# Kernel optimization log

Hardware: AMD Instinct MI355X
Metric: run time of the kernel (lower is better)

## Reference

```python
import jax, jax.numpy as jnp
import numpy as np

K = 9          # kernel_size (number of neighbors), dilation=1
EPS_IN = 1e-5  # InstanceNorm2d eps
EPS_NORM = 1e-12  # F.normalize eps


def instance_norm(x):
    # InstanceNorm2d(affine=False): per-sample, per-channel normalization (biased var)
    m = x.mean(axis=(2, 3), keepdims=True)
    v = x.var(axis=(2, 3), keepdims=True)
    return (x - m) * jax.lax.rsqrt(v + EPS_IN)


def conv1x1(x, w, b):
    # x: [B,C,H,W], w: [O,C], b: [O]
    return jnp.einsum('bchw,oc->bohw', x, w) + b[None, :, None, None]


def setup_inputs() -> dict:
    key = jax.random.key(0)
    ks = jax.random.split(key, 5)
    B, C, H, W = 8, 96, 56, 56
    s = lambda fan_in: 1.0 / np.sqrt(fan_in)
    return {
        'x': jax.random.normal(ks[0], (B, C, H, W), jnp.float32),
        'fc1_w': jax.random.normal(ks[1], (C, C), jnp.float32) * s(C),
        'fc1_b': jnp.zeros((C,), jnp.float32),
        'gconv_w': jax.random.normal(ks[2], (2 * C, 2 * C), jnp.float32) * s(2 * C),
        'gconv_b': jnp.zeros((2 * C,), jnp.float32),
        'fc2_w': jax.random.normal(ks[3], (C, 2 * C), jnp.float32) * s(2 * C),
        'fc2_b': jnp.zeros((C,), jnp.float32),
    }


def reference(x, fc1_w, fc1_b, gconv_w, gconv_b, fc2_w, fc2_b):
    B, C, H, W = x.shape
    N = H * W
    shortcut = x

    # fc1: Conv2d 1x1 + InstanceNorm2d
    h = instance_norm(conv1x1(x, fc1_w, fc1_b))

    # flatten spatial -> nodes: [B,N,C]
    feats = h.reshape(B, C, N).transpose(0, 2, 1)

    # DenseDilatedKnnGraph: l2-normalize features, squared-euclidean pairwise distance, top-k nearest
    nrm = feats / jnp.maximum(jnp.linalg.norm(feats, axis=-1, keepdims=True), EPS_NORM)
    sq = jnp.sum(nrm * nrm, axis=-1)                       # [B,N]
    dist = sq[:, :, None] - 2.0 * jnp.einsum('bnc,bmc->bnm', nrm, nrm) + sq[:, None, :]
    _, nn_idx = jax.lax.top_k(-dist, K)                    # [B,N,K] neighbor indices (edge_index[0])

    # EdgeConv2d: x_i = center features, x_j = gathered neighbor features (unnormalized fc1 output)
    x_i = feats[:, :, None, :]                             # [B,N,1,C]
    x_j = jax.vmap(lambda f, i: f[i])(feats, nn_idx)       # [B,N,K,C]
    edge = jnp.concatenate(
        [jnp.broadcast_to(x_i, x_j.shape), x_j - x_i], axis=-1)  # [B,N,K,2C]

    # BasicConv([2C, 2C], act='relu', norm=None): conv1x1 + bias + relu, then max over neighbors
    e = jax.nn.relu(jnp.einsum('bnkc,oc->bnko', edge, gconv_w) + gconv_b)
    agg = e.max(axis=2)                                    # [B,N,2C]
    g = agg.transpose(0, 2, 1).reshape(B, 2 * C, H, W)

    # fc2: Conv2d 1x1 (2C->C) + InstanceNorm2d, residual
    out = instance_norm(conv1x1(g, fc2_w, fc2_b)) + shortcut
    return out
```

## Files before the change

kernel.cpp:

```cpp
#include <hip/hip_runtime.h>
#include <float.h>

#define BQ 8
#define CHN 96
#define NP 3136
#define KNN 9
#define C2 192
#define NT 196
#define MCH 4
#define TPC (NT/MCH)
#define NFRAG 9
#define NLIST 16

typedef __attribute__((ext_vector_type(8))) short bf16x8;
typedef __attribute__((ext_vector_type(4))) float f32x4;

__device__ inline ushort f2bf(float x) {
  unsigned u = __float_as_uint(x);
  return (ushort)((u + 0x7FFFu + ((u >> 16) & 1u)) >> 16);
}
__device__ inline float bf2f(ushort h) { return __uint_as_float((unsigned)h << 16); }

__global__ __launch_bounds__(256) void k1_conv1(const float* __restrict__ x,
    const float* __restrict__ w, const float* __restrict__ bias, float* __restrict__ h) {
  __shared__ float sw[CHN * CHN];
  __shared__ float sx[CHN][64];
  int b = blockIdx.y;
  int n0 = blockIdx.x * 64;
  int tid = threadIdx.x;
  for (int i = tid; i < CHN * CHN; i += 256) sw[i] = w[i];
  const float* xb = x + (size_t)b * CHN * NP + n0;
  for (int i = tid; i < CHN * 64; i += 256) {
    int c = i >> 6, nn = i & 63;
    sx[c][nn] = xb[(size_t)c * NP + nn];
  }
  __syncthreads();
  int nn = tid & 63;
  int o0 = (tid >> 6) * 24;
  float acc[24];
#pragma unroll
  for (int j = 0; j < 24; ++j) acc[j] = 0.f;
  for (int c = 0; c < CHN; ++c) {
    float xv = sx[c][nn];
#pragma unroll
    for (int j = 0; j < 24; ++j) acc[j] = fmaf(sw[(o0 + j) * CHN + c], xv, acc[j]);
  }
  float* hb = h + (size_t)b * CHN * NP + n0;
#pragma unroll
  for (int j = 0; j < 24; ++j) hb[(size_t)(o0 + j) * NP + nn] = acc[j] + bias[o0 + j];
}

__global__ __launch_bounds__(256) void k2_stats(const float* __restrict__ src,
                                                float* __restrict__ stat) {
  int bo = blockIdx.x;
  const float* p = src + (size_t)bo * NP;
  float s = 0.f, ss = 0.f;
  for (int i = threadIdx.x; i < NP; i += 256) { float v = p[i]; s += v; ss = fmaf(v, v, ss); }
#pragma unroll
  for (int off = 32; off; off >>= 1) { s += __shfl_down(s, off); ss += __shfl_down(ss, off); }
  __shared__ float as[4], ass[4];
  int wv = threadIdx.x >> 6;
  if ((threadIdx.x & 63) == 0) { as[wv] = s; ass[wv] = ss; }
  __syncthreads();
  if (threadIdx.x == 0) {
    float S = as[0] + as[1] + as[2] + as[3];
    float SS = ass[0] + ass[1] + ass[2] + ass[3];
    float mean = S * (1.f / NP);
    float var = SS * (1.f / NP) - mean * mean;
    if (var < 0.f) var = 0.f;
    stat[bo * 2] = mean;
    stat[bo * 2 + 1] = 1.f / sqrtf(var + 1e-5f);
  }
}

__global__ __launch_bounds__(256) void k3_norm(const float* __restrict__ h,
    const float* __restrict__ stat, float* __restrict__ feats, float* __restrict__ nrm,
    float* __restrict__ sq) {
  __shared__ float tile[CHN][33];
  __shared__ float part[8][32];
  __shared__ float sinv[32];
  int b = blockIdx.y, n0 = blockIdx.x * 32;
  int tid = threadIdx.x;
  for (int i = tid; i < CHN * 32; i += 256) {
    int c = i >> 5, nn = i & 31;
    float m = stat[(b * CHN + c) * 2];
    float r = stat[(b * CHN + c) * 2 + 1];
    tile[c][nn] = (h[((size_t)(b * CHN + c)) * NP + n0 + nn] - m) * r;
  }
  __syncthreads();
  int nn = tid & 31, sub = tid >> 5;
  float ss = 0.f;
#pragma unroll
  for (int j = 0; j < 12; ++j) { float f = tile[sub * 12 + j][nn]; ss = fmaf(f, f, ss); }
  part[sub][nn] = ss;
  __syncthreads();
  if (tid < 32) {
    float S = 0.f;
#pragma unroll
    for (int w = 0; w < 8; ++w) S += part[w][tid];
    float norm = sqrtf(S);
    sinv[tid] = 1.f / fmaxf(norm, 1e-12f);
  }
  __syncthreads();
  float inv = sinv[nn];
  float ss2 = 0.f;
#pragma unroll
  for (int j = 0; j < 12; ++j) { float f = tile[sub * 12 + j][nn] * inv; ss2 = fmaf(f, f, ss2); }
  part[sub][nn] = ss2;
  __syncthreads();
  if (tid < 32) {
    float S = 0.f;
#pragma unroll
    for (int w = 0; w < 8; ++w) S += part[w][tid];
    sq[(size_t)b * NP + n0 + tid] = S;
  }
  for (int i = tid; i < 32 * CHN; i += 256) {
    int nn2 = i / CHN, c = i - nn2 * CHN;
    float f = tile[c][nn2];
    size_t o = ((size_t)b * NP + n0 + nn2) * CHN + c;
    feats[o] = f;
    nrm[o] = f * sinv[nn2];
  }
}

__global__ __launch_bounds__(256) void k3b_prep(const float* __restrict__ nrm,
    ushort* __restrict__ ast, ushort* __restrict__ bst) {
  int b = blockIdx.y, t = blockIdx.x;
  int tid = threadIdx.x;
  const float* nb = nrm + (size_t)b * NP * CHN;
  ushort* ao = ast + (((size_t)b * NT + t) * NFRAG) * 512;
  for (int e = tid; e < NFRAG * 512; e += 256) {
    int f = e >> 9, l = (e >> 3) & 63, j = e & 7;
    int part = f / 3, sl = f - part * 3;
    int c = sl * 32 + (l >> 4) * 8 + j;
    int m = t * 16 + (l & 15);
    float xv = nb[(size_t)m * CHN + c];
    ushort hh = f2bf(xv);
    float rm = xv - bf2f(hh);
    ushort md = f2bf(rm);
    ushort v = (part == 0) ? hh : (part == 1) ? md : f2bf(rm - bf2f(md));
    ao[e] = v;
  }
  ushort* bo = bst + (((size_t)b * NT + t) * NFRAG) * 512;
  for (int e = tid; e < NFRAG * 512; e += 256) {
    int f = e >> 9, l = (e >> 3) & 63, j = e & 7;
    int part = f / 3, sl = f - part * 3;
    int c = sl * 32 + (l >> 4) * 8 + j;
    int n = t * 16 + (l & 15);
    float y = -2.f * nb[(size_t)n * CHN + c];
    ushort hh = f2bf(y);
    float rm = y - bf2f(hh);
    ushort md = f2bf(rm);
    ushort v = (part == 0) ? hh : (part == 1) ? md : f2bf(rm - bf2f(md));
    bo[e] = v;
  }
}

#define CSWAP(vI, iI, vJ, iJ) do { \
    bool _s = (vJ) < (vI); \
    float _fa = _s ? (vJ) : (vI); float _fb = _s ? (vI) : (vJ); \
    int _ia = _s ? (iJ) : (iI); int _ib = _s ? (iI) : (iJ); \
    (vI) = _fa; (vJ) = _fb; (iI) = _ia; (iJ) = _ib; \
  } while (0)

__global__ __launch_bounds__(256) void k4_mfma(
    const ushort* __restrict__ ast, const ushort* __restrict__ bst,
    const float* __restrict__ sq, float* __restrict__ pd, int* __restrict__ pi,
    int chunk0) {
  int b = blockIdx.z, chunk = blockIdx.y + chunk0, ng = blockIdx.x;
  int wave = threadIdx.x >> 6, lane = threadIdx.x & 63;
  int tn = ng * 4 + wave;

  __shared__ ushort lds_b[4 * NFRAG * 512];
  {
    const bf16x8* bp = (const bf16x8*)(bst + (((size_t)b * NT + tn) * NFRAG) * 512);
    bf16x8* dst = (bf16x8*)(lds_b + wave * (NFRAG * 512));
#pragma unroll
    for (int f = 0; f < NFRAG; ++f) dst[f * 64 + lane] = bp[f * 64 + lane];
  }
  const bf16x8* bl = (const bf16x8*)(lds_b + wave * (NFRAG * 512));

  const float* sqb = sq + (size_t)b * NP;
  const ushort* astb = ast + ((size_t)b * NT) * (NFRAG * 512);
  int t0 = chunk * TPC;
  const size_t TS = (size_t)NFRAG * 512;

  float tv0 = FLT_MAX, tv1 = FLT_MAX, tv2 = FLT_MAX, tv3 = FLT_MAX, tv4 = FLT_MAX;
  float tv5 = FLT_MAX, tv6 = FLT_MAX, tv7 = FLT_MAX, tv8 = FLT_MAX;
  int ti0 = 0x7fffffff, ti1 = 0x7fffffff, ti2 = 0x7fffffff, ti3 = 0x7fffffff;
  int ti4 = 0x7fffffff, ti5 = 0x7fffffff, ti6 = 0x7fffffff, ti7 = 0x7fffffff;
  int ti8 = 0x7fffffff;

  for (int tl = 0; tl < TPC; ++tl) {
    const bf16x8* ap = (const bf16x8*)(astb + (size_t)(t0 + tl) * TS);
    bf16x8 aH0 = ap[0 * 64 + lane], aH1 = ap[1 * 64 + lane], aH2 = ap[2 * 64 + lane];
    bf16x8 aM0 = ap[3 * 64 + lane], aM1 = ap[4 * 64 + lane], aM2 = ap[5 * 64 + lane];
    bf16x8 aL0 = ap[6 * 64 + lane], aL1 = ap[7 * 64 + lane], aL2 = ap[8 * 64 + lane];
    int mbase = (t0 + tl) * 16 + ((lane >> 4) << 2);
    float4 sqv = *(const float4*)(sqb + mbase);
    f32x4 acc0 = {0.f, 0.f, 0.f, 0.f}, acc1 = {0.f, 0.f, 0.f, 0.f};
    f32x4 acc2 = {0.f, 0.f, 0.f, 0.f}, acc3 = {0.f, 0.f, 0.f, 0.f};
#pragma unroll
    for (int s = 0; s < 3; ++s) {
      bf16x8 aH = (s == 0) ? aH0 : (s == 1) ? aH1 : aH2;
      bf16x8 aM = (s == 0) ? aM0 : (s == 1) ? aM1 : aM2;
      bf16x8 aL = (s == 0) ? aL0 : (s == 1) ? aL1 : aL2;
      bf16x8 bH = bl[(0 + s) * 64 + lane];
      bf16x8 bM = bl[(3 + s) * 64 + lane];
      bf16x8 bL = bl[(6 + s) * 64 + lane];
      acc0 = __builtin_amdgcn_mfma_f32_16x16x32_bf16(aH, bH, acc0, 0, 0, 0);
      acc1 = __builtin_amdgcn_mfma_f32_16x16x32_bf16(aM, bH, acc1, 0, 0, 0);
      acc2 = __builtin_amdgcn_mfma_f32_16x16x32_bf16(aL, bH, acc2, 0, 0, 0);
      acc3 = __builtin_amdgcn_mfma_f32_16x16x32_bf16(aH, bM, acc3, 0, 0, 0);
      acc2 = __builtin_amdgcn_mfma_f32_16x16x32_bf16(aH, bL, acc2, 0, 0, 0);
      acc3 = __builtin_amdgcn_mfma_f32_16x16x32_bf16(aM, bM, acc3, 0, 0, 0);
    }
#pragma unroll
    for (int r = 0; r < 4; ++r) {
      float d = (((acc1[r] + acc3[r]) + acc2[r]) + acc0[r]) + sqv[r];
      int m = mbase + r;
      if (d < tv8) {
        tv8 = d; ti8 = m;
        CSWAP(tv7, ti7, tv8, ti8);
        CSWAP(tv6, ti6, tv7, ti7);
        CSWAP(tv5, ti5, tv6, ti6);
        CSWAP(tv4, ti4, tv5, ti5);
        CSWAP(tv3, ti3, tv4, ti4);
        CSWAP(tv2, ti2, tv3, ti3);
        CSWAP(tv1, ti1, tv2, ti2);
        CSWAP(tv0, ti0, tv1, ti1);
      }
    }
  }
  int g = lane >> 4;
  int n = tn * 16 + (lane & 15);
  size_t base = (((size_t)b * NLIST + (chunk * 4 + g)) * NP + n) * (size_t)KNN;
  pd[base + 0] = tv0; pi[base + 0] = ti0;
  pd[base + 1] = tv1; pi[base + 1] = ti1;
  pd[base + 2] = tv2; pi[base + 2] = ti2;
  pd[base + 3] = tv3; pi[base + 3] = ti3;
  pd[base + 4] = tv4; pi[base + 4] = ti4;
  pd[base + 5] = tv5; pi[base + 5] = ti5;
  pd[base + 6] = tv6; pi[base + 6] = ti6;
  pd[base + 7] = tv7; pi[base + 7] = ti7;
  pd[base + 8] = tv8; pi[base + 8] = ti8;
}

#define ARGMIN4(e0, j0, e1, j1, e2, j2, e3, j3, DW, IW, W0, W1, W2, W3) \
  bool _l01 = ((e0) < (e1)) || ((e0) == (e1) && (j0) < (j1)); \
  float _da = _l01 ? (e0) : (e1); int _ia = _l01 ? (j0) : (j1); \
  bool _l23 = ((e2) < (e3)) || ((e2) == (e3) && (j2) < (j3)); \
  float _db = _l23 ? (e2) : (e3); int _ib = _l23 ? (j2) : (j3); \
  bool _lab = (_da < _db) || (_da == _db && _ia < _ib); \
  float DW = _lab ? _da : _db; int IW = _lab ? _ia : _ib; \
  bool W0 = _lab && _l01, W1 = _lab && !_l01, W2 = !_lab && _l23, W3 = !_lab && !_l23;

__global__ __launch_bounds__(256) void k4b_merge(const float* __restrict__ pd,
    const int* __restrict__ pi, int* __restrict__ nidx) {
  __shared__ float ld_d[256][KNN];
  __shared__ int   ld_i[256][KNN];
  int tid = threadIdx.x;
  int gid = blockIdx.x * 256 + tid;
  int q = gid >> 2, s = gid & 3;
  int b = q / NP, n = q - b * NP;
  size_t b0 = (((size_t)b * NLIST + (s * 4 + 0)) * NP + n) * (size_t)KNN;
  size_t b1 = (((size_t)b * NLIST + (s * 4 + 1)) * NP + n) * (size_t)KNN;
  size_t b2 = (((size_t)b * NLIST + (s * 4 + 2)) * NP + n) * (size_t)KNN;
  size_t b3 = (((size_t)b * NLIST + (s * 4 + 3)) * NP + n) * (size_t)KNN;
  int p0 = 0, p1 = 0, p2 = 0, p3 = 0;
  float d0 = pd[b0], d1 = pd[b1], d2 = pd[b2], d3 = pd[b3];
  int i0 = pi[b0], i1 = pi[b1], i2 = pi[b2], i3 = pi[b3];
#pragma unroll
  for (int k = 0; k < KNN; ++k) {
    ARGMIN4(d0, i0, d1, i1, d2, i2, d3, i3, dw, iw, w0, w1, w2, w3);
    ld_d[tid][k] = dw; ld_i[tid][k] = iw;
    if (w0) { ++p0; bool ok = p0 < KNN; d0 = ok ? pd[b0 + p0] : FLT_MAX; i0 = ok ? pi[b0 + p0] : 0x7fffffff; }
    if (w1) { ++p1; bool ok = p1 < KNN; d1 = ok ? pd[b1 + p1] : FLT_MAX; i1 = ok ? pi[b1 + p1] : 0x7fffffff; }
    if (w2) { ++p2; bool ok = p2 < KNN; d2 = ok ? pd[b2 + p2] : FLT_MAX; i2 = ok ? pi[b2 + p2] : 0x7fffffff; }
    if (w3) { ++p3; bool ok = p3 < KNN; d3 = ok ? pd[b3 + p3] : FLT_MAX; i3 = ok ? pi[b3 + p3] : 0x7fffffff; }
  }
  __syncthreads();
  if (s == 0) {
    int h0 = 0, h1 = 0, h2 = 0, h3 = 0;
    float e0 = ld_d[tid][0], e1 = ld_d[tid + 1][0], e2 = ld_d[tid + 2][0], e3 = ld_d[tid + 3][0];
    int j0 = ld_i[tid][0], j1 = ld_i[tid + 1][0], j2 = ld_i[tid + 2][0], j3 = ld_i[tid + 3][0];
    int* op = nidx + (size_t)q * KNN;
#pragma unroll
    for (int k = 0; k < KNN; ++k) {
      ARGMIN4(e0, j0, e1, j1, e2, j2, e3, j3, dw, iw, w0, w1, w2, w3);
      op[k] = iw;
      if (w0) { ++h0; bool ok = h0 < KNN; e0 = ok ? ld_d[tid][h0] : FLT_MAX; j0 = ok ? ld_i[tid][h0] : 0x7fffffff; }
      if (w1) { ++h1; bool ok = h1 < KNN; e1 = ok ? ld_d[tid + 1][h1] : FLT_MAX; j1 = ok ? ld_i[tid + 1][h1] : 0x7fffffff; }
      if (w2) { ++h2; bool ok = h2 < KNN; e2 = ok ? ld_d[tid + 2][h2] : FLT_MAX; j2 = ok ? ld_i[tid + 2][h2] : 0x7fffffff; }
      if (w3) { ++h3; bool ok = h3 < KNN; e3 = ok ? ld_d[tid + 3][h3] : FLT_MAX; j3 = ok ? ld_i[tid + 3][h3] : 0x7fffffff; }
    }
  }
}

__global__ __launch_bounds__(256) void k5_au(const float* __restrict__ feats,
    const float* __restrict__ gw, const float* __restrict__ gb,
    float* __restrict__ a, float* __restrict__ u) {
  __shared__ float sf[32][97];
  __shared__ float swc[64 * C2];
  int b = blockIdx.y, n0 = blockIdx.x * 32;
  int tid = threadIdx.x;
  for (int i = tid; i < 32 * CHN; i += 256) {
    int nn = i / CHN, c = i - nn * CHN;
    sf[nn][c] = feats[((size_t)b * NP + n0 + nn) * CHN + c];
  }
  int nn = tid & 31, sub = tid >> 5;
  for (int oc = 0; oc < 3; ++oc) {
    __syncthreads();
    for (int i = tid; i < 64 * C2; i += 256) swc[i] = gw[(size_t)(oc * 64) * C2 + i];
    __syncthreads();
    float accA[8], accU[8];
#pragma unroll
    for (int j = 0; j < 8; ++j) { accA[j] = 0.f; accU[j] = 0.f; }
    for (int c = 0; c < CHN; ++c) {
      float f = sf[nn][c];
#pragma unroll
      for (int j = 0; j < 8; ++j) {
        float w1 = swc[(sub * 8 + j) * C2 + c];
        float wv2 = swc[(sub * 8 + j) * C2 + 96 + c];
        accA[j] = fmaf(w1 - wv2, f, accA[j]);
        accU[j] = fmaf(wv2, f, accU[j]);
      }
    }
    size_t row = ((size_t)b * NP + n0 + nn) * C2;
#pragma unroll
    for (int j = 0; j < 8; ++j) {
      int o = oc * 64 + sub * 8 + j;
      a[row + o] = accA[j] + gb[o];
      u[row + o] = accU[j];
    }
  }
}

__global__ __launch_bounds__(256) void k6_edge(const float* __restrict__ a,
    const float* __restrict__ u, const int* __restrict__ nidx,
    const float* __restrict__ w2, const float* __restrict__ b2, float* __restrict__ ol) {
  __shared__ float sagg[32][193];
  int b = blockIdx.y, n0 = blockIdx.x * 32;
  int tid = threadIdx.x;
  int wv = tid >> 6, ln = tid & 63;
  for (int p = 0; p < 8; ++p) {
    int nn = wv * 8 + p;
    size_t row = (size_t)b * NP + n0 + nn;
    const int* ip = nidx + row * KNN;
    int idx[KNN];
#pragma unroll
    for (int k = 0; k < KNN; ++k) idx[k] = ip[k];
#pragma unroll
    for (int oo = 0; oo < 3; ++oo) {
      int o = oo * 64 + ln;
      float umax = -FLT_MAX;
#pragma unroll
      for (int k = 0; k < KNN; ++k)
        umax = fmaxf(umax, u[((size_t)b * NP + idx[k]) * C2 + o]);
      float av = a[row * C2 + o];
      sagg[nn][o] = fmaxf(av + umax, 0.f);
    }
  }
  __syncthreads();
  int nn = tid & 31, sub = tid >> 5;
  for (int j = 0; j < 12; ++j) {
    int o2 = sub + 8 * j;
    float acc = b2[o2];
    for (int o = 0; o < C2; ++o) acc = fmaf(w2[o2 * C2 + o], sagg[nn][o], acc);
    ol[((size_t)b * CHN + o2) * NP + n0 + nn] = acc;
  }
}

__global__ __launch_bounds__(256) void k8_final(const float* __restrict__ ol,
    const float* __restrict__ stat, const float* __restrict__ x, float* __restrict__ out) {
  int i = blockIdx.x * 256 + threadIdx.x;
  int bo = i / NP;
  float m = stat[bo * 2], r = stat[bo * 2 + 1];
  out[i] = fmaf(ol[i] - m, r, x[i]);
}

extern "C" void kernel_launch(void* const* d_in, const int* in_sizes, int n_in,
                              void* d_out, int out_size, void* d_ws, size_t ws_size,
                              hipStream_t stream) {
  const float* x   = (const float*)d_in[0];
  const float* f1w = (const float*)d_in[1];
  const float* f1b = (const float*)d_in[2];
  const float* gw  = (const float*)d_in[3];
  const float* gb  = (const float*)d_in[4];
  const float* f2w = (const float*)d_in[5];
  const float* f2b = (const float*)d_in[6];
  float* out = (float*)d_out;
  char* ws = (char*)d_ws;

  constexpr size_t SZ_MAT = (size_t)BQ * CHN * NP * 4;
  constexpr size_t SZ_STR = (size_t)BQ * NT * NFRAG * 512 * 2;
  constexpr size_t SZ_PL  = (size_t)BQ * NLIST * NP * KNN * 4;
  constexpr size_t OFF_H   = 0;
  constexpr size_t OFF_PD  = 0;
  constexpr size_t OFF_PI  = OFF_PD + SZ_PL;
  constexpr size_t OFF_A   = 0;
  constexpr size_t OFF_AST = 2 * SZ_PL;
  constexpr size_t OFF_BST = OFF_AST + SZ_STR;
  constexpr size_t OFF_U   = OFF_AST;
  constexpr size_t OFF_NRM = OFF_AST + 2 * SZ_STR;
  constexpr size_t OFF_OL  = OFF_NRM;
  constexpr size_t OFF_FE  = OFF_NRM + SZ_MAT;
  constexpr size_t OFF_SQ  = OFF_FE + SZ_MAT;
  constexpr size_t OFF_ST1 = OFF_SQ + (size_t)BQ * NP * 4;
  constexpr size_t OFF_ST2 = OFF_ST1 + (size_t)BQ * CHN * 2 * 4;
  constexpr size_t OFF_NI  = OFF_ST2 + (size_t)BQ * CHN * 2 * 4;

  float* h   = (float*)(ws + OFF_H);
  float* fe  = (float*)(ws + OFF_FE);
  float* nrm = (float*)(ws + OFF_NRM);
  float* sq  = (float*)(ws + OFF_SQ);
  float* st1 = (float*)(ws + OFF_ST1);
  float* st2 = (float*)(ws + OFF_ST2);
  int*   ni  = (int*)(ws + OFF_NI);
  ushort* ast = (ushort*)(ws + OFF_AST);
  ushort* bst = (ushort*)(ws + OFF_BST);
  float* pd  = (float*)(ws + OFF_PD);
  int*   pi  = (int*)(ws + OFF_PI);
  float* aA  = (float*)(ws + OFF_A);
  float* uU  = (float*)(ws + OFF_U);
  float* ol  = (float*)(ws + OFF_OL);

  k1_conv1<<<dim3(NP / 64, BQ), 256, 0, stream>>>(x, f1w, f1b, h);
  k2_stats<<<dim3(BQ * CHN), 256, 0, stream>>>(h, st1);
  k3_norm<<<dim3(NP / 32, BQ), 256, 0, stream>>>(h, st1, fe, nrm, sq);
  k3b_prep<<<dim3(NT, BQ), 256, 0, stream>>>(nrm, ast, bst);
  k4_mfma<<<dim3(NT / 4, MCH, BQ), 256, 0, stream>>>(ast, bst, sq, pd, pi, 0);
  k4b_merge<<<dim3(BQ * NP * 4 / 256), 256, 0, stream>>>(pd, pi, ni);
  k5_au<<<dim3(NP / 32, BQ), 256, 0, stream>>>(fe, gw, gb, aA, uU);
  k6_edge<<<dim3(NP / 32, BQ), 256, 0, stream>>>(aA, uU, ni, f2w, f2b, ol);
  k2_stats<<<dim3(BQ * CHN), 256, 0, stream>>>(ol, st2);
  k8_final<<<dim3(BQ * CHN * NP / 256), 256, 0, stream>>>(ol, st2, x, out);
}
```

Measured before the change: 437.5 us.

## Derive negated-doubled B fragments from A on load, remap blocks, prioritize MFMA

```diff
diff --git a/kernel.cpp b/kernel.cpp
--- a/kernel.cpp
+++ b/kernel.cpp
@@ -14,6 +14,7 @@
 
 typedef __attribute__((ext_vector_type(8))) short bf16x8;
 typedef __attribute__((ext_vector_type(4))) float f32x4;
+typedef __attribute__((ext_vector_type(4))) unsigned int u32x4;
 
 __device__ inline ushort f2bf(float x) {
   unsigned u = __float_as_uint(x);
@@ -124,7 +125,7 @@
 }
 
 __global__ __launch_bounds__(256) void k3b_prep(const float* __restrict__ nrm,
-    ushort* __restrict__ ast, ushort* __restrict__ bst) {
+    ushort* __restrict__ ast) {
   int b = blockIdx.y, t = blockIdx.x;
   int tid = threadIdx.x;
   const float* nb = nrm + (size_t)b * NP * CHN;
@@ -141,19 +142,6 @@
     ushort v = (part == 0) ? hh : (part == 1) ? md : f2bf(rm - bf2f(md));
     ao[e] = v;
   }
-  ushort* bo = bst + (((size_t)b * NT + t) * NFRAG) * 512;
-  for (int e = tid; e < NFRAG * 512; e += 256) {
-    int f = e >> 9, l = (e >> 3) & 63, j = e & 7;
-    int part = f / 3, sl = f - part * 3;
-    int c = sl * 32 + (l >> 4) * 8 + j;
-    int n = t * 16 + (l & 15);
-    float y = -2.f * nb[(size_t)n * CHN + c];
-    ushort hh = f2bf(y);
-    float rm = y - bf2f(hh);
-    ushort md = f2bf(rm);
-    ushort v = (part == 0) ? hh : (part == 1) ? md : f2bf(rm - bf2f(md));
-    bo[e] = v;
-  }
 }
 
 #define CSWAP(vI, iI, vJ, iJ) do { \
@@ -163,20 +151,30 @@
     (vI) = _fa; (vJ) = _fb; (iI) = _ia; (iJ) = _ib; \
   } while (0)
 
+__device__ inline bf16x8 neg2x(bf16x8 v) {
+  u32x4 w = __builtin_bit_cast(u32x4, v);
+#pragma unroll
+  for (int i = 0; i < 4; ++i) w[i] = (w[i] ^ 0x80008000u) + 0x00800080u;
+  return __builtin_bit_cast(bf16x8, w);
+}
+
 __global__ __launch_bounds__(256) void k4_mfma(
-    const ushort* __restrict__ ast, const ushort* __restrict__ bst,
-    const float* __restrict__ sq, float* __restrict__ pd, int* __restrict__ pi,
-    int chunk0) {
-  int b = blockIdx.z, chunk = blockIdx.y + chunk0, ng = blockIdx.x;
+    const ushort* __restrict__ ast, const float* __restrict__ sq,
+    float* __restrict__ pd, int* __restrict__ pi) {
+  int id = blockIdx.x;
+  int g8 = id & 7, r = id >> 3;
+  int ng = r % 49, gd = r / 49;
+  int group = gd * 8 + g8;
+  int chunk = group & 3, b = group >> 2;
   int wave = threadIdx.x >> 6, lane = threadIdx.x & 63;
   int tn = ng * 4 + wave;
 
   __shared__ ushort lds_b[4 * NFRAG * 512];
   {
-    const bf16x8* bp = (const bf16x8*)(bst + (((size_t)b * NT + tn) * NFRAG) * 512);
+    const bf16x8* bp = (const bf16x8*)(ast + (((size_t)b * NT + tn) * NFRAG) * 512);
     bf16x8* dst = (bf16x8*)(lds_b + wave * (NFRAG * 512));
 #pragma unroll
-    for (int f = 0; f < NFRAG; ++f) dst[f * 64 + lane] = bp[f * 64 + lane];
+    for (int f = 0; f < NFRAG; ++f) dst[f * 64 + lane] = neg2x(bp[f * 64 + lane]);
   }
   const bf16x8* bl = (const bf16x8*)(lds_b + wave * (NFRAG * 512));
 
@@ -200,6 +198,7 @@
     float4 sqv = *(const float4*)(sqb + mbase);
     f32x4 acc0 = {0.f, 0.f, 0.f, 0.f}, acc1 = {0.f, 0.f, 0.f, 0.f};
     f32x4 acc2 = {0.f, 0.f, 0.f, 0.f}, acc3 = {0.f, 0.f, 0.f, 0.f};
+    __builtin_amdgcn_s_setprio(1);
 #pragma unroll
     for (int s = 0; s < 3; ++s) {
       bf16x8 aH = (s == 0) ? aH0 : (s == 1) ? aH1 : aH2;
@@ -215,10 +214,11 @@
       acc2 = __builtin_amdgcn_mfma_f32_16x16x32_bf16(aH, bL, acc2, 0, 0, 0);
       acc3 = __builtin_amdgcn_mfma_f32_16x16x32_bf16(aM, bM, acc3, 0, 0, 0);
     }
-#pragma unroll
-    for (int r = 0; r < 4; ++r) {
-      float d = (((acc1[r] + acc3[r]) + acc2[r]) + acc0[r]) + sqv[r];
-      int m = mbase + r;
+    __builtin_amdgcn_s_setprio(0);
+#pragma unroll
+    for (int r2 = 0; r2 < 4; ++r2) {
+      float d = (((acc1[r2] + acc3[r2]) + acc2[r2]) + acc0[r2]) + sqv[r2];
+      int m = mbase + r2;
       if (d < tv8) {
         tv8 = d; ti8 = m;
         CSWAP(tv7, ti7, tv8, ti8);
@@ -400,7 +400,6 @@
   constexpr size_t OFF_PI  = OFF_PD + SZ_PL;
   constexpr size_t OFF_A   = 0;
   constexpr size_t OFF_AST = 2 * SZ_PL;
-  constexpr size_t OFF_BST = OFF_AST + SZ_STR;
   constexpr size_t OFF_U   = OFF_AST;
   constexpr size_t OFF_NRM = OFF_AST + 2 * SZ_STR;
   constexpr size_t OFF_OL  = OFF_NRM;
@@ -418,7 +417,6 @@
   float* st2 = (float*)(ws + OFF_ST2);
   int*   ni  = (int*)(ws + OFF_NI);
   ushort* ast = (ushort*)(ws + OFF_AST);
-  ushort* bst = (ushort*)(ws + OFF_BST);
   float* pd  = (float*)(ws + OFF_PD);
   int*   pi  = (int*)(ws + OFF_PI);
   float* aA  = (float*)(ws + OFF_A);
@@ -428,8 +426,8 @@
   k1_conv1<<<dim3(NP / 64, BQ), 256, 0, stream>>>(x, f1w, f1b, h);
   k2_stats<<<dim3(BQ * CHN), 256, 0, stream>>>(h, st1);
   k3_norm<<<dim3(NP / 32, BQ), 256, 0, stream>>>(h, st1, fe, nrm, sq);
-  k3b_prep<<<dim3(NT, BQ), 256, 0, stream>>>(nrm, ast, bst);
-  k4_mfma<<<dim3(NT / 4, MCH, BQ), 256, 0, stream>>>(ast, bst, sq, pd, pi, 0);
+  k3b_prep<<<dim3(NT, BQ), 256, 0, stream>>>(nrm, ast);
+  k4_mfma<<<dim3((NT / 4) * MCH * BQ), 256, 0, stream>>>(ast, sq, pd, pi);
   k4b_merge<<<dim3(BQ * NP * 4 / 256), 256, 0, stream>>>(pd, pi, ni);
   k5_au<<<dim3(NP / 32, BQ), 256, 0, stream>>>(fe, gw, gb, aA, uU);
   k6_edge<<<dim3(NP / 32, BQ), 256, 0, stream>>>(aA, uU, ni, f2w, f2b, ol);
```

Measured after the change: 414.2 us. 1.06x faster.
